# Kernel optimization log

Hardware: AMD Instinct MI355X
Metric: run time of the kernel (lower is better)

The kernel has to match this reference:

```python
import jax, jax.numpy as jnp
import numpy as np

D = 1024   # d_model
H = 16     # n_heads
S = 2048   # seq_len
HD = D // H  # head_dim = 64
B = 1


def setup_inputs() -> dict:
    key = jax.random.key(0)
    ks = jax.random.split(key, 10)
    s = 0.02
    return {
        "x": jax.random.normal(ks[0], (B, S * D), dtype=jnp.float32),
        "Wq": jax.random.normal(ks[1], (D, D), dtype=jnp.float32) * s,
        "bq": jnp.zeros((D,), dtype=jnp.float32),
        "Wk": jax.random.normal(ks[2], (D, D), dtype=jnp.float32) * s,
        "bk": jnp.zeros((D,), dtype=jnp.float32),
        "Wv": jax.random.normal(ks[3], (D, D), dtype=jnp.float32) * s,
        "bv": jnp.zeros((D,), dtype=jnp.float32),
        "Wo": jax.random.normal(ks[4], (D, D), dtype=jnp.float32) * s,
        "bo": jnp.zeros((D,), dtype=jnp.float32),
        "rel_table": jax.random.normal(ks[5], (2 * S - 1, HD), dtype=jnp.float32),
    }


def reference(x, Wq, bq, Wk, bk, Wv, bv, Wo, bo, rel_table):
    b = x.shape[0]
    x3 = x.reshape(b, S, D)
    # projections; split into heads -> [b, H, S, HD]
    def heads(t):
        return t.reshape(b, S, H, HD).transpose(0, 2, 1, 3)
    Q = heads(x3 @ Wq + bq)
    K = heads(x3 @ Wk + bk)
    V = heads(x3 @ Wv + bv)

    scores = jnp.einsum('bhid,bhjd->bhij', Q, K) / np.sqrt(HD).astype(np.float32)

    # relative position index: clamp(i - j + S - 1, 0, 2S-2)
    pos = jnp.arange(S)
    idx = jnp.clip(pos[:, None] - pos[None, :] + S - 1, 0, 2 * S - 2)  # [S, S]
    # contract Q with the raw table once, then gather per (i, j)
    # (same math as einsum('bhid,ijd->bhij', Q, table[idx]) but avoids [S,S,HD])
    qrel = jnp.einsum('bhid,rd->bhir', Q, rel_table)          # [b, H, S, 2S-1]
    rel_scores = jnp.take_along_axis(qrel, idx[None, None, :, :], axis=-1)  # [b,H,S,S]

    attn = jax.nn.softmax(scores + rel_scores, axis=-1)
    # dropout is identity in eval mode
    out = jnp.einsum('bhij,bhjd->bhid', attn, V)              # [b, H, S, HD]
    out = out.transpose(0, 2, 1, 3).reshape(b, S, D)
    return (out @ Wo + bo).reshape(b, -1)
```

## Files before the change

kernel.cpp:

```cpp
#include <hip/hip_runtime.h>
#include <hip/hip_bf16.h>

#define SEQ 2048
#define DM  1024
#define NH  16
#define HDM 64

typedef __hip_bfloat16 bf16;
typedef __bf16 bhalf8 __attribute__((ext_vector_type(8)));
typedef float floatx4 __attribute__((ext_vector_type(4)));

__device__ __forceinline__ void async_cp16(const void* g, void* l) {
  __builtin_amdgcn_global_load_lds(
      (const __attribute__((address_space(1))) void*)g,
      (__attribute__((address_space(3))) void*)l, 16, 0, 0);
}

__global__ __launch_bounds__(256) void prep(
    const float* __restrict__ x, const float* __restrict__ T,
    const float* __restrict__ W0, const float* __restrict__ W1,
    const float* __restrict__ W2, const float* __restrict__ W3,
    bf16* __restrict__ xbf, bf16* __restrict__ Tbf, bf16* __restrict__ WtBase)
{
  __shared__ float tile[64][69];
  const int b = blockIdx.x;
  const int tid = threadIdx.x;
  if (b < 2048) {
    int c = b * 256 + tid;
    float4 v = *(const float4*)&x[(size_t)c * 4];
    union { bf16 h[4]; float2 f; } u;
    u.h[0] = __float2bfloat16(v.x); u.h[1] = __float2bfloat16(v.y);
    u.h[2] = __float2bfloat16(v.z); u.h[3] = __float2bfloat16(v.w);
    *(float2*)&xbf[(size_t)c * 4] = u.f;
  } else if (b < 2304) {
    int ct = (b - 2048) * 256 + tid;
    union { bf16 h[4]; float2 f; } u;
#pragma unroll
    for (int e = 0; e < 4; ++e) {
      int se = ct * 4 + e;
      if (se >= 4095 * 64) se -= 64;
      u.h[e] = __float2bfloat16(T[se]);
    }
    *(float2*)&Tbf[(size_t)ct * 4] = u.f;
  } else {
    int tb = b - 2304;
    int z = tb >> 8, rem = tb & 255;
    const float* W = (z == 0) ? W0 : (z == 1) ? W1 : (z == 2) ? W2 : W3;
    bf16* Wt = WtBase + (size_t)z * DM * DM;
    const int kb = (rem >> 4) * 64, nb = (rem & 15) * 64;
    const int r = tid >> 4, c4 = (tid & 15) * 4;
#pragma unroll
    for (int rr = 0; rr < 4; ++rr) {
      float4 v = *(const float4*)&W[(size_t)(kb + rr * 16 + r) * DM + nb + c4];
      tile[rr * 16 + r][c4 + 0] = v.x; tile[rr * 16 + r][c4 + 1] = v.y;
      tile[rr * 16 + r][c4 + 2] = v.z; tile[rr * 16 + r][c4 + 3] = v.w;
    }
    __syncthreads();
    const int w = tid >> 6, l = tid & 63;
#pragma unroll
    for (int i = 0; i < 16; ++i) {
      int n = nb + w * 16 + i;
      Wt[(size_t)n * DM + kb + l] = __float2bfloat16(tile[l][w * 16 + i]);
    }
  }
}

__device__ __forceinline__ void gemm64_core(
    const bf16* __restrict__ A, const bf16* __restrict__ Bt,
    bf16* As, bf16* Bs, int bm, int bn, floatx4 (&acc)[4])
{
  const int tid = threadIdx.x;
  const int lane = tid & 63;
  const int w = tid >> 6;
  const int ln15 = lane & 15, quad = lane >> 4;

  for (int k0 = 0; k0 < DM; k0 += 64) {
    {
      int c = w * 64 + lane;
      int row = c >> 2, col = (c & 3) * 8;
      async_cp16(A  + (size_t)(bm + row) * DM + k0 + col,      As + c * 8);
      async_cp16(A  + (size_t)(bm + row) * DM + k0 + 32 + col, As + 2048 + c * 8);
      async_cp16(Bt + (size_t)(bn + row) * DM + k0 + col,      Bs + c * 8);
      async_cp16(Bt + (size_t)(bn + row) * DM + k0 + 32 + col, Bs + 2048 + c * 8);
    }
    __syncthreads();
#pragma unroll
    for (int kk = 0; kk < 2; ++kk) {
      bhalf8 af = *(bhalf8*)&As[kk * 2048 + (w * 16 + ln15) * 32 + quad * 8];
      bhalf8 bfr[4];
#pragma unroll
      for (int j = 0; j < 4; ++j)
        bfr[j] = *(bhalf8*)&Bs[kk * 2048 + (j * 16 + ln15) * 32 + quad * 8];
#pragma unroll
      for (int j = 0; j < 4; ++j)
        acc[j] = __builtin_amdgcn_mfma_f32_16x16x32_bf16(af, bfr[j], acc[j], 0, 0, 0);
    }
    __syncthreads();
  }
}

__global__ __launch_bounds__(256) void gemm_qkv(
    const bf16* __restrict__ A, const bf16* __restrict__ Wt3,
    const float* __restrict__ bq, const float* __restrict__ bk,
    const float* __restrict__ bv, bf16* __restrict__ outbase)
{
  __shared__ __align__(16) bf16 As[64 * 64];
  __shared__ __align__(16) bf16 Bs[64 * 64];
  const int z = blockIdx.z;
  const bf16* Bt = Wt3 + (size_t)z * DM * DM;
  const float* bias = (z == 0) ? bq : (z == 1) ? bk : bv;
  const float kscale = (z == 1) ? 0.125f : 1.0f;
  bf16* C = outbase + (size_t)z * SEQ * DM;
  const int bm = blockIdx.y * 64, bn = blockIdx.x * 64;
  floatx4 acc[4];
#pragma unroll
  for (int j = 0; j < 4; ++j) acc[j] = (floatx4){0.f, 0.f, 0.f, 0.f};
  gemm64_core(A, Bt, As, Bs, bm, bn, acc);

  const int lane = threadIdx.x & 63;
  const int w = threadIdx.x >> 6;
  const int ln15 = lane & 15, quad = lane >> 4;
#pragma unroll
  for (int j = 0; j < 4; ++j) {
    int col = bn + j * 16 + ln15;
    float bv_ = bias[col];
#pragma unroll
    for (int r = 0; r < 4; ++r) {
      int row = bm + w * 16 + quad * 4 + r;
      float v = (acc[j][r] + bv_) * kscale;
      if (z < 2)
        C[((size_t)(col >> 6) * SEQ + row) * HDM + (col & 63)] = __float2bfloat16(v);
      else
        C[(size_t)col * SEQ + row] = __float2bfloat16(v);
    }
  }
}

__global__ __launch_bounds__(256) void gemm_out(
    const bf16* __restrict__ A, const bf16* __restrict__ Bt,
    const float* __restrict__ bias, float* __restrict__ C)
{
  __shared__ __align__(16) bf16 As[64 * 64];
  __shared__ __align__(16) bf16 Bs[64 * 64];
  const int bm = blockIdx.y * 64, bn = blockIdx.x * 64;
  floatx4 acc[4];
#pragma unroll
  for (int j = 0; j < 4; ++j) acc[j] = (floatx4){0.f, 0.f, 0.f, 0.f};
  gemm64_core(A, Bt, As, Bs, bm, bn, acc);

  const int lane = threadIdx.x & 63;
  const int w = threadIdx.x >> 6;
  const int ln15 = lane & 15, quad = lane >> 4;
#pragma unroll
  for (int j = 0; j < 4; ++j) {
    int col = bn + j * 16 + ln15;
    float bv_ = bias[col];
#pragma unroll
    for (int r = 0; r < 4; ++r) {
      int row = bm + w * 16 + quad * 4 + r;
      C[(size_t)row * DM + col] = acc[j][r] + bv_;
    }
  }
}

__global__ __launch_bounds__(256, 3) void attn_flash(
    const bf16* __restrict__ Q, const bf16* __restrict__ K,
    const bf16* __restrict__ Vt, const bf16* __restrict__ Tb,
    bf16* __restrict__ Opart, float* __restrict__ ml)
{
  const int i0   = blockIdx.x * 64;
  const int h    = blockIdx.y;
  const int z    = blockIdx.z;
  const int tid  = threadIdx.x;
  const int lane = tid & 63;
  const int wrow = (tid >> 6) * 16;
  const int ln15 = lane & 15;
  const int quad = lane >> 4;

  __shared__ __align__(16) unsigned char smem[51200];
  bf16*  Ks  = (bf16*)smem;
  bf16*  Vs  = (bf16*)(smem + 8192);
  bf16*  Ts  = (bf16*)(smem + 16384);
  bf16*  Ps  = (bf16*)(smem + 24576);
  float* S2t = (float*)(smem + 33792);
  bf16*  Qs  = (bf16*)(smem + 33792);

  const bf16* Qg = Q  + ((size_t)h * SEQ + i0) * HDM;
  const bf16* Kg = K  + (size_t)h * SEQ * HDM;
  const bf16* Vg = Vt + (size_t)h * HDM * SEQ;

#pragma unroll
  for (int t = 0; t < 2; ++t) {
    int id = tid + t * 256;
    int r = id >> 3, c = (id & 7) * 8;
    *(float4*)&Qs[r * 72 + c] = *(const float4*)&Qg[(size_t)r * HDM + c];
  }
  __syncthreads();

  const bhalf8 aq0 = *(bhalf8*)&Qs[(wrow + ln15) * 72 + quad * 8];
  const bhalf8 aq1 = *(bhalf8*)&Qs[(wrow + ln15) * 72 + quad * 8 + 32];

  floatx4 o[4];
  float mrow[4], lrow[4];
#pragma unroll
  for (int c = 0; c < 4; ++c) o[c] = (floatx4){0.f, 0.f, 0.f, 0.f};
#pragma unroll
  for (int r = 0; r < 4; ++r) { mrow[r] = -1e30f; lrow[r] = 0.f; }

  const int jt0 = z * 16;
  const int rb0 = i0 - jt0 * 64 + SEQ - HDM;
  floatx4 carry[4];
#pragma unroll
  for (int ct = 0; ct < 4; ++ct) {
    const bf16* tr = Tb + (size_t)(rb0 + 64 + ct * 16 + ln15) * HDM + quad * 8;
    bhalf8 b0 = *(const bhalf8*)tr;
    bhalf8 b1 = *(const bhalf8*)(tr + 32);
    floatx4 a = (floatx4){0.f, 0.f, 0.f, 0.f};
    a = __builtin_amdgcn_mfma_f32_16x16x32_bf16(aq0, b0, a, 0, 0, 0);
    a = __builtin_amdgcn_mfma_f32_16x16x32_bf16(aq1, b1, a, 0, 0, 0);
    carry[ct] = a;
  }

  const int r4 = tid >> 2, c8 = (tid & 3) * 8;

  for (int jt = jt0; jt < jt0 + 16; ++jt) {
    const int j0 = jt * 64;
    const int rbase = i0 - j0 + SEQ - HDM;
    __syncthreads();
    async_cp16(Kg + (size_t)(j0 + r4) * HDM + c8,        Ks + tid * 8);
    async_cp16(Kg + (size_t)(j0 + r4) * HDM + 32 + c8,   Ks + 2048 + tid * 8);
    async_cp16(Vg + (size_t)r4 * SEQ + j0 + c8,          Vs + tid * 8);
    async_cp16(Vg + (size_t)r4 * SEQ + j0 + 32 + c8,     Vs + 2048 + tid * 8);
    async_cp16(Tb + (size_t)(rbase + r4) * HDM + c8,     Ts + tid * 8);
    async_cp16(Tb + (size_t)(rbase + r4) * HDM + 32 + c8, Ts + 2048 + tid * 8);
    __syncthreads();

    floatx4 fresh[4];
#pragma unroll
    for (int ct = 0; ct < 4; ++ct) {
      bhalf8 b0 = *(bhalf8*)&Ts[(ct * 16 + ln15) * 32 + quad * 8];
      bhalf8 b1 = *(bhalf8*)&Ts[2048 + (ct * 16 + ln15) * 32 + quad * 8];
      floatx4 a = (floatx4){0.f, 0.f, 0.f, 0.f};
      a = __builtin_amdgcn_mfma_f32_16x16x32_bf16(aq0, b0, a, 0, 0, 0);
      a = __builtin_amdgcn_mfma_f32_16x16x32_bf16(aq1, b1, a, 0, 0, 0);
      fresh[ct] = a;
    }
#pragma unroll
    for (int ct = 0; ct < 4; ++ct) {
      int t = ct * 16 + ln15;
#pragma unroll
      for (int r = 0; r < 4; ++r) {
        int row = wrow + quad * 4 + r;
        if (t >= row) S2t[(row + 63 - t) * 68 + row] = fresh[ct][r];
        else          S2t[(row - 1 - t) * 68 + row] = carry[ct][r];
      }
      carry[ct] = fresh[ct];
    }

    float sc[4][4];
#pragma unroll
    for (int ct = 0; ct < 4; ++ct) {
      floatx4 s2f = *(floatx4*)&S2t[(ct * 16 + ln15) * 68 + wrow + quad * 4];
      bhalf8 b0 = *(bhalf8*)&Ks[(ct * 16 + ln15) * 32 + quad * 8];
      bhalf8 b1 = *(bhalf8*)&Ks[2048 + (ct * 16 + ln15) * 32 + quad * 8];
      floatx4 a = __builtin_amdgcn_mfma_f32_16x16x32_bf16(aq0, b0, s2f, 0, 0, 0);
      a = __builtin_amdgcn_mfma_f32_16x16x32_bf16(aq1, b1, a, 0, 0, 0);
#pragma unroll
      for (int r = 0; r < 4; ++r) sc[ct][r] = a[r];
    }
#pragma unroll
    for (int r = 0; r < 4; ++r) {
      float tm = fmaxf(fmaxf(sc[0][r], sc[1][r]), fmaxf(sc[2][r], sc[3][r]));
      tm = fmaxf(tm, __shfl_xor(tm, 1));
      tm = fmaxf(tm, __shfl_xor(tm, 2));
      tm = fmaxf(tm, __shfl_xor(tm, 4));
      tm = fmaxf(tm, __shfl_xor(tm, 8));
      float mn = fmaxf(mrow[r], tm);
      float alpha = __expf(mrow[r] - mn);
      mrow[r] = mn;
      float rs = 0.f;
#pragma unroll
      for (int ct = 0; ct < 4; ++ct) {
        float p = __expf(sc[ct][r] - mn);
        sc[ct][r] = p;
        rs += p;
      }
      rs += __shfl_xor(rs, 1); rs += __shfl_xor(rs, 2);
      rs += __shfl_xor(rs, 4); rs += __shfl_xor(rs, 8);
      lrow[r] = lrow[r] * alpha + rs;
#pragma unroll
      for (int ct = 0; ct < 4; ++ct) o[ct][r] *= alpha;
    }
#pragma unroll
    for (int ct = 0; ct < 4; ++ct)
#pragma unroll
      for (int r = 0; r < 4; ++r)
        Ps[(wrow + quad * 4 + r) * 72 + ct * 16 + ln15] = __float2bfloat16(sc[ct][r]);

    bhalf8 ap0 = *(bhalf8*)&Ps[(wrow + ln15) * 72 + quad * 8];
    bhalf8 ap1 = *(bhalf8*)&Ps[(wrow + ln15) * 72 + quad * 8 + 32];
#pragma unroll
    for (int ct = 0; ct < 4; ++ct) {
      bhalf8 b0 = *(bhalf8*)&Vs[(ct * 16 + ln15) * 32 + quad * 8];
      bhalf8 b1 = *(bhalf8*)&Vs[2048 + (ct * 16 + ln15) * 32 + quad * 8];
      o[ct] = __builtin_amdgcn_mfma_f32_16x16x32_bf16(ap0, b0, o[ct], 0, 0, 0);
      o[ct] = __builtin_amdgcn_mfma_f32_16x16x32_bf16(ap1, b1, o[ct], 0, 0, 0);
    }
  }

  bf16* Oz = Opart + (size_t)z * SEQ * DM;
#pragma unroll
  for (int r = 0; r < 4; ++r) {
    float inv = 1.f / lrow[r];
    int row = i0 + wrow + quad * 4 + r;
#pragma unroll
    for (int ct = 0; ct < 4; ++ct)
      Oz[(size_t)row * DM + h * HDM + ct * 16 + ln15] =
          __float2bfloat16(o[ct][r] * inv);
    if (ln15 == 0) {
      float* mlp = ml + (((size_t)z * NH + h) * SEQ + row) * 2;
      mlp[0] = mrow[r];
      mlp[1] = lrow[r];
    }
  }
}

__global__ __launch_bounds__(256) void attn_merge(
    const bf16* __restrict__ O0, const bf16* __restrict__ O1,
    const float* __restrict__ ml, bf16* __restrict__ O)
{
  const int i = blockIdx.x;
  const int tid = threadIdx.x;
  __shared__ float w0s[NH], w1s[NH];
  if (tid < NH) {
    const float* p0 = ml + (((size_t)0 * NH + tid) * SEQ + i) * 2;
    const float* p1 = ml + (((size_t)1 * NH + tid) * SEQ + i) * 2;
    float m0 = p0[0], l0 = p0[1], m1 = p1[0], l1 = p1[1];
    float m = fmaxf(m0, m1);
    float a = l0 * __expf(m0 - m), b = l1 * __expf(m1 - m);
    float inv = 1.f / (a + b);
    w0s[tid] = a * inv; w1s[tid] = b * inv;
  }
  __syncthreads();
  const int d = tid * 4;
  const float w0 = w0s[d >> 6], w1 = w1s[d >> 6];
  union { bf16 h[4]; float2 f; } a0, a1, ov;
  a0.f = *(const float2*)&O0[(size_t)i * DM + d];
  a1.f = *(const float2*)&O1[(size_t)i * DM + d];
#pragma unroll
  for (int e = 0; e < 4; ++e)
    ov.h[e] = __float2bfloat16(w0 * __bfloat162float(a0.h[e]) +
                               w1 * __bfloat162float(a1.h[e]));
  *(float2*)&O[(size_t)i * DM + d] = ov.f;
}

extern "C" void kernel_launch(void* const* d_in, const int* in_sizes, int n_in,
                              void* d_out, int out_size, void* d_ws, size_t ws_size,
                              hipStream_t stream) {
  const float* x   = (const float*)d_in[0];
  const float* Wq  = (const float*)d_in[1];
  const float* bq  = (const float*)d_in[2];
  const float* Wk  = (const float*)d_in[3];
  const float* bk  = (const float*)d_in[4];
  const float* Wv  = (const float*)d_in[5];
  const float* bv  = (const float*)d_in[6];
  const float* Wo  = (const float*)d_in[7];
  const float* bo  = (const float*)d_in[8];
  const float* rel = (const float*)d_in[9];
  float* out = (float*)d_out;

  const size_t SD = (size_t)SEQ * DM;
  bf16* qws = (bf16*)d_ws;
  bf16* kws = qws + SD;
  bf16* vws = kws + SD;
  bf16* ows = vws + SD;
  bf16* xbf = ows + SD;
  bf16* wt  = xbf + SD;
  bf16* tbf = wt + 4 * (size_t)DM * DM;
  bf16* opart = tbf + (size_t)4096 * HDM;
  float* ml   = (float*)(opart + 2 * SD);

  prep<<<3328, 256, 0, stream>>>(x, rel, Wq, Wk, Wv, Wo, xbf, tbf, wt);
  gemm_qkv<<<dim3(16, 32, 3), 256, 0, stream>>>(xbf, wt, bq, bk, bv, qws);
  attn_flash<<<dim3(SEQ / 64, NH, 2), 256, 0, stream>>>(qws, kws, vws, tbf,
                                                        opart, ml);
  attn_merge<<<SEQ, 256, 0, stream>>>(opart, opart + SD, ml, ows);
  gemm_out<<<dim3(16, 32), 256, 0, stream>>>(ows, wt + 3 * (size_t)DM * DM, bo, out);
}
```

Measured before the change: 226.7 us.

## Double query rows per attention block to reuse K, V and rel-table tiles

Each attention block now covers 128 query rows instead of 64, with every wave owning two 16-row groups, so each K, V and rel-table tile loaded into LDS feeds twice as much MFMA work. The rel-position scores now span two 64-column diagonals, so a second carry buffer is kept and the skewed scatter into LDS is rewritten row-major with a three-way select. LDS use grows to about 75 KB and register pressure rises, so launch bounds drop to 2 blocks per CU and the grid is halved to 512 blocks, which lowers occupancy and parallelism.

```diff
diff --git a/kernel.cpp b/kernel.cpp
--- a/kernel.cpp
+++ b/kernel.cpp
@@ -163,62 +163,77 @@
   }
 }
 
-__global__ __launch_bounds__(256, 3) void attn_flash(
+__global__ __launch_bounds__(256, 2) void attn_flash(
     const bf16* __restrict__ Q, const bf16* __restrict__ K,
     const bf16* __restrict__ Vt, const bf16* __restrict__ Tb,
     bf16* __restrict__ Opart, float* __restrict__ ml)
 {
-  const int i0   = blockIdx.x * 64;
+  const int i0   = blockIdx.x * 128;
   const int h    = blockIdx.y;
   const int z    = blockIdx.z;
   const int tid  = threadIdx.x;
   const int lane = tid & 63;
-  const int wrow = (tid >> 6) * 16;
+  const int wrow = (tid >> 6) * 32;
   const int ln15 = lane & 15;
   const int quad = lane >> 4;
 
-  __shared__ __align__(16) unsigned char smem[51200];
+  __shared__ __align__(16) unsigned char smem[76800];
   bf16*  Ks  = (bf16*)smem;
   bf16*  Vs  = (bf16*)(smem + 8192);
   bf16*  Ts  = (bf16*)(smem + 16384);
   bf16*  Ps  = (bf16*)(smem + 24576);
-  float* S2t = (float*)(smem + 33792);
-  bf16*  Qs  = (bf16*)(smem + 33792);
+  float* S2c = (float*)(smem + 43008);
+  bf16*  Qs  = (bf16*)(smem + 43008);
 
   const bf16* Qg = Q  + ((size_t)h * SEQ + i0) * HDM;
   const bf16* Kg = K  + (size_t)h * SEQ * HDM;
   const bf16* Vg = Vt + (size_t)h * HDM * SEQ;
 
 #pragma unroll
-  for (int t = 0; t < 2; ++t) {
+  for (int t = 0; t < 4; ++t) {
     int id = tid + t * 256;
     int r = id >> 3, c = (id & 7) * 8;
     *(float4*)&Qs[r * 72 + c] = *(const float4*)&Qg[(size_t)r * HDM + c];
   }
   __syncthreads();
 
-  const bhalf8 aq0 = *(bhalf8*)&Qs[(wrow + ln15) * 72 + quad * 8];
-  const bhalf8 aq1 = *(bhalf8*)&Qs[(wrow + ln15) * 72 + quad * 8 + 32];
-
-  floatx4 o[4];
-  float mrow[4], lrow[4];
-#pragma unroll
-  for (int c = 0; c < 4; ++c) o[c] = (floatx4){0.f, 0.f, 0.f, 0.f};
-#pragma unroll
-  for (int r = 0; r < 4; ++r) { mrow[r] = -1e30f; lrow[r] = 0.f; }
+  bhalf8 aq[2][2];
+#pragma unroll
+  for (int g = 0; g < 2; ++g) {
+    aq[g][0] = *(bhalf8*)&Qs[(wrow + g * 16 + ln15) * 72 + quad * 8];
+    aq[g][1] = *(bhalf8*)&Qs[(wrow + g * 16 + ln15) * 72 + quad * 8 + 32];
+  }
+
+  floatx4 o[2][4];
+  float mrow[2][4], lrow[2][4];
+#pragma unroll
+  for (int g = 0; g < 2; ++g)
+#pragma unroll
+    for (int c = 0; c < 4; ++c) {
+      o[g][c] = (floatx4){0.f, 0.f, 0.f, 0.f};
+      mrow[g][c] = -1e30f; lrow[g][c] = 0.f;
+    }
 
   const int jt0 = z * 16;
   const int rb0 = i0 - jt0 * 64 + SEQ - HDM;
-  floatx4 carry[4];
+  floatx4 c1[2][4], c2[2][4];
 #pragma unroll
   for (int ct = 0; ct < 4; ++ct) {
-    const bf16* tr = Tb + (size_t)(rb0 + 64 + ct * 16 + ln15) * HDM + quad * 8;
-    bhalf8 b0 = *(const bhalf8*)tr;
-    bhalf8 b1 = *(const bhalf8*)(tr + 32);
-    floatx4 a = (floatx4){0.f, 0.f, 0.f, 0.f};
-    a = __builtin_amdgcn_mfma_f32_16x16x32_bf16(aq0, b0, a, 0, 0, 0);
-    a = __builtin_amdgcn_mfma_f32_16x16x32_bf16(aq1, b1, a, 0, 0, 0);
-    carry[ct] = a;
+    const bf16* t1 = Tb + (size_t)(rb0 + 64 + ct * 16 + ln15) * HDM + quad * 8;
+    const bf16* t2 = Tb + (size_t)(rb0 + 128 + ct * 16 + ln15) * HDM + quad * 8;
+    bhalf8 b10 = *(const bhalf8*)t1, b11 = *(const bhalf8*)(t1 + 32);
+    bhalf8 b20 = *(const bhalf8*)t2, b21 = *(const bhalf8*)(t2 + 32);
+#pragma unroll
+    for (int g = 0; g < 2; ++g) {
+      floatx4 a = (floatx4){0.f, 0.f, 0.f, 0.f};
+      a = __builtin_amdgcn_mfma_f32_16x16x32_bf16(aq[g][0], b10, a, 0, 0, 0);
+      a = __builtin_amdgcn_mfma_f32_16x16x32_bf16(aq[g][1], b11, a, 0, 0, 0);
+      c1[g][ct] = a;
+      a = (floatx4){0.f, 0.f, 0.f, 0.f};
+      a = __builtin_amdgcn_mfma_f32_16x16x32_bf16(aq[g][0], b20, a, 0, 0, 0);
+      a = __builtin_amdgcn_mfma_f32_16x16x32_bf16(aq[g][1], b21, a, 0, 0, 0);
+      c2[g][ct] = a;
+    }
   }
 
   const int r4 = tid >> 2, c8 = (tid & 3) * 8;
@@ -227,102 +242,130 @@
     const int j0 = jt * 64;
     const int rbase = i0 - j0 + SEQ - HDM;
     __syncthreads();
-    async_cp16(Kg + (size_t)(j0 + r4) * HDM + c8,        Ks + tid * 8);
-    async_cp16(Kg + (size_t)(j0 + r4) * HDM + 32 + c8,   Ks + 2048 + tid * 8);
-    async_cp16(Vg + (size_t)r4 * SEQ + j0 + c8,          Vs + tid * 8);
-    async_cp16(Vg + (size_t)r4 * SEQ + j0 + 32 + c8,     Vs + 2048 + tid * 8);
-    async_cp16(Tb + (size_t)(rbase + r4) * HDM + c8,     Ts + tid * 8);
+    async_cp16(Kg + (size_t)(j0 + r4) * HDM + c8,         Ks + tid * 8);
+    async_cp16(Kg + (size_t)(j0 + r4) * HDM + 32 + c8,    Ks + 2048 + tid * 8);
+    async_cp16(Vg + (size_t)r4 * SEQ + j0 + c8,           Vs + tid * 8);
+    async_cp16(Vg + (size_t)r4 * SEQ + j0 + 32 + c8,      Vs + 2048 + tid * 8);
+    async_cp16(Tb + (size_t)(rbase + r4) * HDM + c8,      Ts + tid * 8);
     async_cp16(Tb + (size_t)(rbase + r4) * HDM + 32 + c8, Ts + 2048 + tid * 8);
     __syncthreads();
 
-    floatx4 fresh[4];
+    floatx4 fresh[2][4];
 #pragma unroll
     for (int ct = 0; ct < 4; ++ct) {
       bhalf8 b0 = *(bhalf8*)&Ts[(ct * 16 + ln15) * 32 + quad * 8];
       bhalf8 b1 = *(bhalf8*)&Ts[2048 + (ct * 16 + ln15) * 32 + quad * 8];
-      floatx4 a = (floatx4){0.f, 0.f, 0.f, 0.f};
-      a = __builtin_amdgcn_mfma_f32_16x16x32_bf16(aq0, b0, a, 0, 0, 0);
-      a = __builtin_amdgcn_mfma_f32_16x16x32_bf16(aq1, b1, a, 0, 0, 0);
-      fresh[ct] = a;
-    }
+#pragma unroll
+      for (int g = 0; g < 2; ++g) {
+        floatx4 a = (floatx4){0.f, 0.f, 0.f, 0.f};
+        a = __builtin_amdgcn_mfma_f32_16x16x32_bf16(aq[g][0], b0, a, 0, 0, 0);
+        a = __builtin_amdgcn_mfma_f32_16x16x32_bf16(aq[g][1], b1, a, 0, 0, 0);
+        fresh[g][ct] = a;
+      }
+    }
+#pragma unroll
+    for (int g = 0; g < 2; ++g)
+#pragma unroll
+      for (int ct = 0; ct < 4; ++ct) {
+        int t = ct * 16 + ln15;
+#pragma unroll
+        for (int r = 0; r < 4; ++r) {
+          int row = wrow + g * 16 + quad * 4 + r;
+          int cf = row + 63 - t, cm = row - 1 - t, cl = row - 65 - t;
+          if ((unsigned)cf < 64u)      S2c[row * 66 + cf] = fresh[g][ct][r];
+          else if ((unsigned)cm < 64u) S2c[row * 66 + cm] = c1[g][ct][r];
+          else                         S2c[row * 66 + cl] = c2[g][ct][r];
+        }
+        c2[g][ct] = c1[g][ct];
+        c1[g][ct] = fresh[g][ct];
+      }
+
+    floatx4 sc[2][4];
 #pragma unroll
     for (int ct = 0; ct < 4; ++ct) {
-      int t = ct * 16 + ln15;
-#pragma unroll
-      for (int r = 0; r < 4; ++r) {
-        int row = wrow + quad * 4 + r;
-        if (t >= row) S2t[(row + 63 - t) * 68 + row] = fresh[ct][r];
-        else          S2t[(row - 1 - t) * 68 + row] = carry[ct][r];
-      }
-      carry[ct] = fresh[ct];
-    }
-
-    float sc[4][4];
-#pragma unroll
-    for (int ct = 0; ct < 4; ++ct) {
-      floatx4 s2f = *(floatx4*)&S2t[(ct * 16 + ln15) * 68 + wrow + quad * 4];
       bhalf8 b0 = *(bhalf8*)&Ks[(ct * 16 + ln15) * 32 + quad * 8];
       bhalf8 b1 = *(bhalf8*)&Ks[2048 + (ct * 16 + ln15) * 32 + quad * 8];
-      floatx4 a = __builtin_amdgcn_mfma_f32_16x16x32_bf16(aq0, b0, s2f, 0, 0, 0);
-      a = __builtin_amdgcn_mfma_f32_16x16x32_bf16(aq1, b1, a, 0, 0, 0);
-#pragma unroll
-      for (int r = 0; r < 4; ++r) sc[ct][r] = a[r];
-    }
-#pragma unroll
-    for (int r = 0; r < 4; ++r) {
-      float tm = fmaxf(fmaxf(sc[0][r], sc[1][r]), fmaxf(sc[2][r], sc[3][r]));
-      tm = fmaxf(tm, __shfl_xor(tm, 1));
-      tm = fmaxf(tm, __shfl_xor(tm, 2));
-      tm = fmaxf(tm, __shfl_xor(tm, 4));
-      tm = fmaxf(tm, __shfl_xor(tm, 8));
-      float mn = fmaxf(mrow[r], tm);
-      float alpha = __expf(mrow[r] - mn);
-      mrow[r] = mn;
-      float rs = 0.f;
-#pragma unroll
-      for (int ct = 0; ct < 4; ++ct) {
-        float p = __expf(sc[ct][r] - mn);
-        sc[ct][r] = p;
-        rs += p;
-      }
-      rs += __shfl_xor(rs, 1); rs += __shfl_xor(rs, 2);
-      rs += __shfl_xor(rs, 4); rs += __shfl_xor(rs, 8);
-      lrow[r] = lrow[r] * alpha + rs;
-#pragma unroll
-      for (int ct = 0; ct < 4; ++ct) o[ct][r] *= alpha;
-    }
-#pragma unroll
-    for (int ct = 0; ct < 4; ++ct)
-#pragma unroll
-      for (int r = 0; r < 4; ++r)
-        Ps[(wrow + quad * 4 + r) * 72 + ct * 16 + ln15] = __float2bfloat16(sc[ct][r]);
-
-    bhalf8 ap0 = *(bhalf8*)&Ps[(wrow + ln15) * 72 + quad * 8];
-    bhalf8 ap1 = *(bhalf8*)&Ps[(wrow + ln15) * 72 + quad * 8 + 32];
+#pragma unroll
+      for (int g = 0; g < 2; ++g) {
+        floatx4 s2f;
+#pragma unroll
+        for (int r = 0; r < 4; ++r)
+          s2f[r] = S2c[(wrow + g * 16 + quad * 4 + r) * 66 + ct * 16 + ln15];
+        floatx4 a = __builtin_amdgcn_mfma_f32_16x16x32_bf16(aq[g][0], b0, s2f, 0, 0, 0);
+        a = __builtin_amdgcn_mfma_f32_16x16x32_bf16(aq[g][1], b1, a, 0, 0, 0);
+        sc[g][ct] = a;
+      }
+    }
+#pragma unroll
+    for (int g = 0; g < 2; ++g)
+#pragma unroll
+      for (int r = 0; r < 4; ++r) {
+        float tm = fmaxf(fmaxf(sc[g][0][r], sc[g][1][r]),
+                         fmaxf(sc[g][2][r], sc[g][3][r]));
+        tm = fmaxf(tm, __shfl_xor(tm, 1));
+        tm = fmaxf(tm, __shfl_xor(tm, 2));
+        tm = fmaxf(tm, __shfl_xor(tm, 4));
+        tm = fmaxf(tm, __shfl_xor(tm, 8));
+        float mn = fmaxf(mrow[g][r], tm);
+        float alpha = __expf(mrow[g][r] - mn);
+        mrow[g][r] = mn;
+        float rs = 0.f;
+#pragma unroll
+        for (int ct = 0; ct < 4; ++ct) {
+          float p = __expf(sc[g][ct][r] - mn);
+          sc[g][ct][r] = p;
+          rs += p;
+        }
+        rs += __shfl_xor(rs, 1); rs += __shfl_xor(rs, 2);
+        rs += __shfl_xor(rs, 4); rs += __shfl_xor(rs, 8);
+        lrow[g][r] = lrow[g][r] * alpha + rs;
+#pragma unroll
+        for (int ct = 0; ct < 4; ++ct) o[g][ct][r] *= alpha;
+      }
+#pragma unroll
+    for (int g = 0; g < 2; ++g)
+#pragma unroll
+      for (int ct = 0; ct < 4; ++ct)
+#pragma unroll
+        for (int r = 0; r < 4; ++r)
+          Ps[(wrow + g * 16 + quad * 4 + r) * 72 + ct * 16 + ln15] =
+              __float2bfloat16(sc[g][ct][r]);
+
+    bhalf8 ap[2][2];
+#pragma unroll
+    for (int g = 0; g < 2; ++g) {
+      ap[g][0] = *(bhalf8*)&Ps[(wrow + g * 16 + ln15) * 72 + quad * 8];
+      ap[g][1] = *(bhalf8*)&Ps[(wrow + g * 16 + ln15) * 72 + quad * 8 + 32];
+    }
 #pragma unroll
     for (int ct = 0; ct < 4; ++ct) {
       bhalf8 b0 = *(bhalf8*)&Vs[(ct * 16 + ln15) * 32 + quad * 8];
       bhalf8 b1 = *(bhalf8*)&Vs[2048 + (ct * 16 + ln15) * 32 + quad * 8];
-      o[ct] = __builtin_amdgcn_mfma_f32_16x16x32_bf16(ap0, b0, o[ct], 0, 0, 0);
-      o[ct] = __builtin_amdgcn_mfma_f32_16x16x32_bf16(ap1, b1, o[ct], 0, 0, 0);
+#pragma unroll
+      for (int g = 0; g < 2; ++g) {
+        o[g][ct] = __builtin_amdgcn_mfma_f32_16x16x32_bf16(ap[g][0], b0, o[g][ct], 0, 0, 0);
+        o[g][ct] = __builtin_amdgcn_mfma_f32_16x16x32_bf16(ap[g][1], b1, o[g][ct], 0, 0, 0);
+      }
     }
   }
 
   bf16* Oz = Opart + (size_t)z * SEQ * DM;
 #pragma unroll
-  for (int r = 0; r < 4; ++r) {
-    float inv = 1.f / lrow[r];
-    int row = i0 + wrow + quad * 4 + r;
-#pragma unroll
-    for (int ct = 0; ct < 4; ++ct)
-      Oz[(size_t)row * DM + h * HDM + ct * 16 + ln15] =
-          __float2bfloat16(o[ct][r] * inv);
-    if (ln15 == 0) {
-      float* mlp = ml + (((size_t)z * NH + h) * SEQ + row) * 2;
-      mlp[0] = mrow[r];
-      mlp[1] = lrow[r];
-    }
-  }
+  for (int g = 0; g < 2; ++g)
+#pragma unroll
+    for (int r = 0; r < 4; ++r) {
+      float inv = 1.f / lrow[g][r];
+      int row = i0 + wrow + g * 16 + quad * 4 + r;
+#pragma unroll
+      for (int ct = 0; ct < 4; ++ct)
+        Oz[(size_t)row * DM + h * HDM + ct * 16 + ln15] =
+            __float2bfloat16(o[g][ct][r] * inv);
+      if (ln15 == 0) {
+        float* mlp = ml + (((size_t)z * NH + h) * SEQ + row) * 2;
+        mlp[0] = mrow[g][r];
+        mlp[1] = lrow[g][r];
+      }
+    }
 }
 
 __global__ __launch_bounds__(256) void attn_merge(
@@ -382,8 +425,8 @@
 
   prep<<<3328, 256, 0, stream>>>(x, rel, Wq, Wk, Wv, Wo, xbf, tbf, wt);
   gemm_qkv<<<dim3(16, 32, 3), 256, 0, stream>>>(xbf, wt, bq, bk, bv, qws);
-  attn_flash<<<dim3(SEQ / 64, NH, 2), 256, 0, stream>>>(qws, kws, vws, tbf,
-                                                        opart, ml);
+  attn_flash<<<dim3(SEQ / 128, NH, 2), 256, 0, stream>>>(qws, kws, vws, tbf,
+                                                         opart, ml);
   attn_merge<<<SEQ, 256, 0, stream>>>(opart, opart + SD, ml, ows);
   gemm_out<<<dim3(16, 32), 256, 0, stream>>>(ows, wt + 3 * (size_t)DM * DM, bo, out);
 }
```

Measured after the change: 260.3 us. 14.8% more time.
